# Optimization experiments

Measured on AMD Instinct MI355X. Metric: run time of the kernel, lower is better.

The kernel has to match this reference:

```python
import jax, jax.numpy as jnp
import numpy as np

D = 512        # input_dim
T = 64         # n_trees
DEPTH = 3
NI = 2 ** DEPTH - 1   # 7 internal nodes
NL = 2 ** DEPTH       # 8 leaves
PPT = NI * D + NI + NL * 2   # params per tree
TOT = PPT * T + T            # + tree_weights
HID = 64


def setup_inputs() -> dict:
    key = jax.random.key(0)
    ks = jax.random.split(key, 10)
    w = lambda k, s: jax.random.normal(k, s, jnp.float32) * 0.05  # xavier-ish small gain
    return {
        "X_train": jax.random.normal(ks[0], (8192, D), jnp.float32),
        "X_test": jax.random.normal(ks[1], (32768, D), jnp.float32),
        "y_train": jax.random.randint(ks[2], (8192,), 0, 2, jnp.int64),
        "W1": w(ks[3], (HID, D)), "b1": jnp.zeros(HID), "g1": jnp.ones(HID), "be1": jnp.zeros(HID),
        "W2": w(ks[4], (HID, HID)), "b2": jnp.zeros(HID),
        "H1": w(ks[5], (2 * HID, HID)), "hb1": jnp.zeros(2 * HID),
        "g2": jnp.ones(2 * HID), "be2": jnp.zeros(2 * HID),
        "H2": w(ks[6], (2 * HID, 2 * HID)), "hb2": jnp.zeros(2 * HID),
        "H3": w(ks[7], (TOT, 2 * HID)), "hb3": jnp.zeros(TOT),
    }


def _ln(x, g, b, eps=1e-5):
    m = x.mean(-1, keepdims=True)
    v = ((x - m) ** 2).mean(-1, keepdims=True)
    return (x - m) / jnp.sqrt(v + eps) * g + b


def reference(X_train, X_test, y_train, W1, b1, g1, be1, W2, b2,
              H1, hb1, g2, be2, H2, hb2, H3, hb3):
    # --- hypernet: data encoder + param generator (Dropout is eval=identity) ---
    h = jax.nn.relu(_ln(X_train @ W1.T + b1, g1, be1))
    h = jax.nn.relu(h @ W2.T + b2)
    c = h.mean(axis=0)                              # [HID] context
    u = jax.nn.relu(_ln(c @ H1.T + hb1, g2, be2))
    u = jax.nn.relu(u @ H2.T + hb2)
    params = u @ H3.T + hb3                         # [TOT]

    # --- parse per-tree params (sequential layout) ---
    rows = params[: T * PPT].reshape(T, PPT)
    sw = rows[:, : NI * D].reshape(T, NI, D)        # split weights
    sb = rows[:, NI * D: NI * D + NI]               # split bias [T, NI]
    ll = rows[:, NI * D + NI:].reshape(T, NL, 2)    # leaf logits
    tw = params[T * PPT:]                           # tree weights [T]

    # --- soft decision trees, all trees/nodes batched ---
    # sigmoid split prob for every (sample, tree, internal node); temperature=1
    p = jax.nn.sigmoid(jnp.einsum('bd,tnd->btn', X_test, sw) + sb[None])  # [B,T,NI]
    B = X_test.shape[0]
    lp = jnp.ones((B, T, 1), X_test.dtype)
    for d in range(DEPTH):                          # unrolled fixed-depth traversal
        s = 2 ** d - 1                              # heap offset of level d
        pd = p[:, :, s: s + 2 ** d]                 # [B,T,2^d]
        lp = jnp.stack([lp * (1 - pd), lp * pd], axis=-1).reshape(B, T, 2 ** (d + 1))
    # original code adds leaf contributions twice (main loop + cleanup loop)
    lp = lp * 2.0                                   # [B,T,NL]

    leaf_dist = jax.nn.softmax(ll, axis=-1)         # [T,NL,2]
    out_t = jnp.einsum('btl,tlc->btc', lp, leaf_dist)
    w = jax.nn.softmax(tw, axis=0)                  # [T]
    return jnp.einsum('btc,t->bc', out_t, w)        # [B,2]
```

## Files before the change

### kernel.cpp

```cpp
#include <hip/hip_runtime.h>
#include <hip/hip_bf16.h>

#define DD 512
#define HIDN 64
#define NTREE 64
#define NIN 7
#define PPTC 3607
#define TOTP 230912
#define SWROWS 448

typedef __attribute__((ext_vector_type(8))) short bf16x8;
typedef __attribute__((ext_vector_type(4))) float f32x4;
typedef __attribute__((ext_vector_type(8))) _Float16 h16x8;

__device__ __forceinline__ unsigned short f2bf(float f) {
  unsigned u = __float_as_uint(f);
  unsigned r = (u + 0x7FFFu + ((u >> 16) & 1u)) >> 16;
  return (unsigned short)r;
}
__device__ __forceinline__ float sigmoidf_(float x) {
  return 1.0f / (1.0f + __expf(-x));
}
__device__ __forceinline__ uint2 pack_bf16x4(float4 v) {
  uint2 pk;
  pk.x = (unsigned)f2bf(v.x) | ((unsigned)f2bf(v.y) << 16);
  pk.y = (unsigned)f2bf(v.z) | ((unsigned)f2bf(v.w) << 16);
  return pk;
}
__device__ __forceinline__ bf16x8 cvt8(float4 a, float4 b) {
  unsigned u0, u1, u2, u3;
  asm("v_cvt_pk_bf16_f32 %0, %1, %2" : "=v"(u0) : "v"(a.x), "v"(a.y));
  asm("v_cvt_pk_bf16_f32 %0, %1, %2" : "=v"(u1) : "v"(a.z), "v"(a.w));
  asm("v_cvt_pk_bf16_f32 %0, %1, %2" : "=v"(u2) : "v"(b.x), "v"(b.y));
  asm("v_cvt_pk_bf16_f32 %0, %1, %2" : "=v"(u3) : "v"(b.z), "v"(b.w));
  union { unsigned u[4]; bf16x8 v; } r;
  r.u[0] = u0; r.u[1] = u1; r.u[2] = u2; r.u[3] = u3;
  return r.v;
}

__global__ __launch_bounds__(256) void k_train(
    const float* __restrict__ Xtr, const float* __restrict__ W1,
    const float* __restrict__ b1, const float* __restrict__ g1,
    const float* __restrict__ be1, const float* __restrict__ W2,
    const float* __restrict__ b2, float* __restrict__ c_part)
{
  __shared__ __align__(16) char smem[37888];
  char* Xc  = smem;
  char* W1c = smem + 8192;
  char* Hl  = smem + 24576;
  char* W2l = smem + 28672;
  float* lnb = (float*)(smem + 36864);
  float* cp  = (float*)(smem + 37376);

  const int tid = threadIdx.x;
  const int lane = tid & 63;
  const int wv = tid >> 6;
  const int l15 = lane & 15;
  const int gq = lane >> 4;
  const int wm = wv >> 1;
  const int wn = wv & 1;
  const int rb0 = blockIdx.x * 32;

  const float4* X4g = (const float4*)Xtr;
  const float4* W4g = (const float4*)W1;

#pragma unroll
  for (int s = 0; s < 4; ++s) {
    int fidx = tid + s * 256;
    int n = fidx >> 4, kq = fidx & 15;
    float4 v = ((const float4*)W2)[n * 16 + kq];
    uint2 pk = pack_bf16x4(v);
    int off = n * 128 + kq * 8; off ^= (n & 7) << 4;
    *(uint2*)(W2l + off) = pk;
  }

  int xga[4], xo[4];
#pragma unroll
  for (int s = 0; s < 4; ++s) {
    int f = tid + s * 256;
    int m = f >> 5, kq = f & 31;
    xga[s] = (rb0 + m) * 128 + kq;
    xo[s] = (m * 256 + kq * 8) ^ ((m & 7) << 4);
  }
  int wga[8], wo[8];
#pragma unroll
  for (int s = 0; s < 8; ++s) {
    int f = tid + s * 256;
    int n = f >> 5, kq = f & 31;
    wga[s] = n * 128 + kq;
    wo[s] = (n * 256 + kq * 8) ^ ((n & 7) << 4);
  }

  f32x4 acc1[2];
#pragma unroll
  for (int nt = 0; nt < 2; ++nt) { f32x4 z = {0.f,0.f,0.f,0.f}; acc1[nt] = z; }

  float4 xr[4], wr[8];
#pragma unroll
  for (int s = 0; s < 4; ++s) xr[s] = X4g[xga[s]];
#pragma unroll
  for (int s = 0; s < 8; ++s) wr[s] = W4g[wga[s]];

  for (int kc = 0; kc < 4; ++kc) {
    __syncthreads();
#pragma unroll
    for (int s = 0; s < 4; ++s) *(uint2*)(Xc + xo[s]) = pack_bf16x4(xr[s]);
#pragma unroll
    for (int s = 0; s < 8; ++s) *(uint2*)(W1c + wo[s]) = pack_bf16x4(wr[s]);
    if (kc < 3) {
      int ko = (kc + 1) * 32;
#pragma unroll
      for (int s = 0; s < 4; ++s) xr[s] = X4g[xga[s] + ko];
#pragma unroll
      for (int s = 0; s < 8; ++s) wr[s] = W4g[wga[s] + ko];
    }
    __syncthreads();
#pragma unroll
    for (int ks = 0; ks < 4; ++ks) {
      int arow = wm * 16 + l15;
      int aoff = (arow * 256 + ks * 64 + gq * 16) ^ ((arow & 7) << 4);
      bf16x8 afr = *(const bf16x8*)(Xc + aoff);
#pragma unroll
      for (int nt = 0; nt < 2; ++nt) {
        int brow = wn * 32 + nt * 16 + l15;
        int boff = (brow * 256 + ks * 64 + gq * 16) ^ ((brow & 7) << 4);
        bf16x8 bfr = *(const bf16x8*)(W1c + boff);
        acc1[nt] = __builtin_amdgcn_mfma_f32_16x16x32_bf16(afr, bfr, acc1[nt], 0, 0, 0);
      }
    }
  }

  float b1v[2], g1v[2], be1v[2], b2v[2];
#pragma unroll
  for (int nt = 0; nt < 2; ++nt) {
    int c = wn * 32 + nt * 16 + l15;
    b1v[nt] = b1[c]; g1v[nt] = g1[c]; be1v[nt] = be1[c]; b2v[nt] = b2[c];
  }
  float yv[2][4], s_[4], q_[4];
#pragma unroll
  for (int i = 0; i < 4; ++i) {
    float s = 0.f, q = 0.f;
#pragma unroll
    for (int nt = 0; nt < 2; ++nt) {
      float y = acc1[nt][i] + b1v[nt];
      yv[nt][i] = y; s += y; q += y * y;
    }
    s_[i] = s; q_[i] = q;
  }
#pragma unroll
  for (int off = 1; off < 16; off <<= 1) {
#pragma unroll
    for (int i = 0; i < 4; ++i) {
      s_[i] += __shfl_xor(s_[i], off);
      q_[i] += __shfl_xor(q_[i], off);
    }
  }
  if (l15 == 0) {
#pragma unroll
    for (int i = 0; i < 4; ++i) {
      int row = wm * 16 + gq * 4 + i;
      float2 sv; sv.x = s_[i]; sv.y = q_[i];
      *(float2*)(lnb + (row * 2 + wn) * 2) = sv;
    }
  }
  __syncthreads();
#pragma unroll
  for (int i = 0; i < 4; ++i) {
    int row = wm * 16 + gq * 4 + i;
    float2 e0 = *(float2*)(lnb + (row * 2 + 0) * 2);
    float2 e1 = *(float2*)(lnb + (row * 2 + 1) * 2);
    float m = (e0.x + e1.x) * (1.0f / 64.0f);
    float var = (e0.y + e1.y) * (1.0f / 64.0f) - m * m;
    float rstd = rsqrtf(var + 1e-5f);
#pragma unroll
    for (int nt = 0; nt < 2; ++nt) {
      float h = (yv[nt][i] - m) * rstd * g1v[nt] + be1v[nt];
      h = fmaxf(h, 0.0f);
      int col = wn * 32 + nt * 16 + l15;
      int off2 = (row * 128 + col * 2) ^ ((row & 7) << 4);
      *(unsigned short*)(Hl + off2) = f2bf(h);
    }
  }
  __syncthreads();

  f32x4 acc2[2];
#pragma unroll
  for (int nt = 0; nt < 2; ++nt) { f32x4 z = {0.f,0.f,0.f,0.f}; acc2[nt] = z; }
#pragma unroll
  for (int ks = 0; ks < 2; ++ks) {
    int arow = wm * 16 + l15;
    int aoff = (arow * 128 + ks * 64 + gq * 16) ^ ((arow & 7) << 4);
    bf16x8 afr = *(const bf16x8*)(Hl + aoff);
#pragma unroll
    for (int nt = 0; nt < 2; ++nt) {
      int brow = wn * 32 + nt * 16 + l15;
      int boff = (brow * 128 + ks * 64 + gq * 16) ^ ((brow & 7) << 4);
      bf16x8 bfr = *(const bf16x8*)(W2l + boff);
      acc2[nt] = __builtin_amdgcn_mfma_f32_16x16x32_bf16(afr, bfr, acc2[nt], 0, 0, 0);
    }
  }
  float cs[2];
#pragma unroll
  for (int nt = 0; nt < 2; ++nt) {
    float s = 0.f;
#pragma unroll
    for (int i = 0; i < 4; ++i) s += fmaxf(acc2[nt][i] + b2v[nt], 0.0f);
    cs[nt] = s;
  }
#pragma unroll
  for (int nt = 0; nt < 2; ++nt) {
    cs[nt] += __shfl_xor(cs[nt], 16);
    cs[nt] += __shfl_xor(cs[nt], 32);
  }
  if (lane < 16) {
#pragma unroll
    for (int nt = 0; nt < 2; ++nt)
      cp[wm * 64 + wn * 32 + nt * 16 + lane] = cs[nt];
  }
  __syncthreads();
  if (tid < 64) c_part[blockIdx.x * 64 + tid] = cp[tid] + cp[64 + tid];
}

__global__ __launch_bounds__(256) void k_head(
    const float* __restrict__ c_part,
    const float* __restrict__ H1, const float* __restrict__ hb1,
    const float* __restrict__ g2, const float* __restrict__ be2,
    const float* __restrict__ H2, const float* __restrict__ hb2,
    float* __restrict__ u2out)
{
  __shared__ float part[256];
  __shared__ float clds[64];
  __shared__ float u1lds[128];
  __shared__ float red[8];
  int tid = threadIdx.x;
  {
    int col = tid & 63, g = tid >> 6;
    float s0 = 0.f, s1 = 0.f, s2 = 0.f, s3 = 0.f;
    int b0 = g * 64;
    for (int b = 0; b < 64; b += 4) {
      s0 += c_part[(b0 + b + 0) * 64 + col];
      s1 += c_part[(b0 + b + 1) * 64 + col];
      s2 += c_part[(b0 + b + 2) * 64 + col];
      s3 += c_part[(b0 + b + 3) * 64 + col];
    }
    part[tid] = (s0 + s1) + (s2 + s3);
  }
  __syncthreads();
  if (tid < 64)
    clds[tid] = (part[tid] + part[64 + tid] + part[128 + tid] + part[192 + tid]) * (1.0f / 8192.0f);
  __syncthreads();
  float acc = 0.f;
  if (tid < 128) {
    float a0 = 0.f, a1 = 0.f, a2 = 0.f, a3 = 0.f;
    for (int k = 0; k < 64; k += 4) {
      a0 += clds[k + 0] * H1[tid * 64 + k + 0];
      a1 += clds[k + 1] * H1[tid * 64 + k + 1];
      a2 += clds[k + 2] * H1[tid * 64 + k + 2];
      a3 += clds[k + 3] * H1[tid * 64 + k + 3];
    }
    acc = hb1[tid] + ((a0 + a1) + (a2 + a3));
  }
  float s = acc, q = acc * acc;
#pragma unroll
  for (int off = 1; off < 64; off <<= 1) { s += __shfl_xor(s, off); q += __shfl_xor(q, off); }
  int wv = tid >> 6;
  if ((tid & 63) == 0) { red[wv * 2] = s; red[wv * 2 + 1] = q; }
  __syncthreads();
  float S = red[0] + red[2], Q = red[1] + red[3];
  float m = S * (1.0f / 128.0f);
  float var = Q * (1.0f / 128.0f) - m * m;
  float rstd = rsqrtf(var + 1e-5f);
  if (tid < 128)
    u1lds[tid] = fmaxf((acc - m) * rstd * g2[tid] + be2[tid], 0.0f);
  __syncthreads();
  if (tid < 128) {
    float c0 = 0.f, c1 = 0.f, c2 = 0.f, c3 = 0.f;
    for (int k = 0; k < 128; k += 4) {
      c0 += u1lds[k + 0] * H2[tid * 128 + k + 0];
      c1 += u1lds[k + 1] * H2[tid * 128 + k + 1];
      c2 += u1lds[k + 2] * H2[tid * 128 + k + 2];
      c3 += u1lds[k + 3] * H2[tid * 128 + k + 3];
    }
    u2out[tid] = fmaxf(hb2[tid] + ((c0 + c1) + (c2 + c3)), 0.0f);
  }
}

__global__ __launch_bounds__(256) void k_params(
    const float* __restrict__ H3, const float* __restrict__ hb3,
    const float* __restrict__ u2,
    unsigned short* __restrict__ Bsw, float* __restrict__ sb,
    float* __restrict__ ll, float* __restrict__ tw)
{
  __shared__ float u2l[128];
  int tid = threadIdx.x;
  if (tid < 128) u2l[tid] = u2[tid];
  __syncthreads();
  int row = blockIdx.x * 64 + (tid >> 2);
  int sub = tid & 3;
  float acc = 0.0f;
  const float4* H4 = (const float4*)H3;
#pragma unroll
  for (int j = 0; j < 8; ++j) {
    int f = j * 4 + sub;
    float4 v = H4[row * 32 + f];
    acc += v.x * u2l[f * 4] + v.y * u2l[f * 4 + 1] + v.z * u2l[f * 4 + 2] + v.w * u2l[f * 4 + 3];
  }
  acc += __shfl_xor(acc, 1);
  acc += __shfl_xor(acc, 2);
  if (sub == 0) {
    float val = acc + hb3[row];
    if (row >= 230848) {
      tw[row - 230848] = val;
    } else {
      int t = row / PPTC;
      int r = row - t * PPTC;
      if (r < 3584) {
        int n = r >> 9, d = r & 511;
        Bsw[(t * 7 + n) * 512 + d] = f2bf(val);
      } else if (r < 3591) {
        sb[t * 7 + (r - 3584)] = val;
      } else {
        ll[t * 16 + (r - 3591)] = val;
      }
    }
  }
}

__global__ __launch_bounds__(512) void k_test(
    const float* __restrict__ Xt, const unsigned short* __restrict__ Bsw,
    const float* __restrict__ sb, const float* __restrict__ ll,
    const float* __restrict__ tw, float* __restrict__ out)
{
  __shared__ __align__(16) char smem[64256];
  char* Bb0 = smem;
  char* Bb1 = smem + 28672;
  char* Pl  = smem;
  float* qlds = (float*)(smem + 57344);
  float* sbl  = (float*)(smem + 61440);
  float* outl = (float*)(smem + 63232);

  const int tid = threadIdx.x;
  const int lane = tid & 63;
  const int wv = tid >> 6;
  const int l15 = lane & 15;
  const int gq = lane >> 4;
  const int wm = wv >> 2;
  const int wn = wv & 3;
  const int bm0 = blockIdx.x * 128;
  const bool btail = (tid < 256);

  int bg[4], bo[4];
#pragma unroll
  for (int s = 0; s < 4; ++s) {
    int idx = tid + s * 512;
    int n = idx >> 2, part = idx & 3;
    bg[s] = n * 64 + part;
    bo[s] = (n * 64 + part * 16) ^ ((n & 7) << 4);
  }
  int abase[4];
#pragma unroll
  for (int mt = 0; mt < 4; ++mt) {
    int row = bm0 + wm * 64 + mt * 16 + l15;
    abase[mt] = row * 128 + gq * 2;
  }
  int boffs[7];
#pragma unroll
  for (int nt = 0; nt < 7; ++nt) {
    int r = wn * 112 + nt * 16 + l15;
    boffs[nt] = (r * 64 + gq * 16) ^ ((r & 7) << 4);
  }

  f32x4 acc[4][7];
#pragma unroll
  for (int mt = 0; mt < 4; ++mt)
#pragma unroll
    for (int nt = 0; nt < 7; ++nt) { f32x4 z = {0.f,0.f,0.f,0.f}; acc[mt][nt] = z; }

  const float4* X4 = (const float4*)Xt;
  const uint4* B4 = (const uint4*)Bsw;

  float4 af[4][2];
  bf16x8 abf[4];
  uint4 br0, br1, br2, br3;

#define LOADA(kt) do { _Pragma("unroll") \
    for (int mt = 0; mt < 4; ++mt) { \
      af[mt][0] = X4[abase[mt] + (kt) * 8]; \
      af[mt][1] = X4[abase[mt] + (kt) * 8 + 1]; } } while (0)
#define CVTA() do { _Pragma("unroll") \
    for (int mt = 0; mt < 4; ++mt) abf[mt] = cvt8(af[mt][0], af[mt][1]); } while (0)
#define LOADB(kt) do { \
    br0 = B4[bg[0] + (kt) * 4]; br1 = B4[bg[1] + (kt) * 4]; \
    br2 = B4[bg[2] + (kt) * 4]; if (btail) br3 = B4[bg[3] + (kt) * 4]; } while (0)
#define STOREB(Bb) do { \
    *(uint4*)((Bb) + bo[0]) = br0; *(uint4*)((Bb) + bo[1]) = br1; \
    *(uint4*)((Bb) + bo[2]) = br2; if (btail) *(uint4*)((Bb) + bo[3]) = br3; } while (0)
#define COMPUTE(Bb) do { _Pragma("unroll") \
    for (int nt = 0; nt < 7; ++nt) { \
      bf16x8 bfr = *(const bf16x8*)((Bb) + boffs[nt]); \
      _Pragma("unroll") \
      for (int mt = 0; mt < 4; ++mt) \
        acc[mt][nt] = __builtin_amdgcn_mfma_f32_16x16x32_bf16(abf[mt], bfr, acc[mt][nt], 0, 0, 0); \
    } } while (0)

  LOADA(0);
  LOADB(0);
  STOREB(Bb0);
  LOADB(1);
  if (tid < 448) sbl[tid] = sb[tid];
  if (tid < 64) {
    int t = tid;
    float x = tw[t];
    float m = x;
#pragma unroll
    for (int off = 1; off < 64; off <<= 1) m = fmaxf(m, __shfl_xor(m, off));
    float e = __expf(x - m);
    float s = e;
#pragma unroll
    for (int off = 1; off < 64; off <<= 1) s += __shfl_xor(s, off);
    float w = e / s;
#pragma unroll
    for (int l = 0; l < 8; ++l) {
      float a = ll[t * 16 + l * 2], b = ll[t * 16 + l * 2 + 1];
      float mm = fmaxf(a, b);
      float e0 = __expf(a - mm), e1 = __expf(b - mm);
      float inv = 2.0f * w / (e0 + e1);
      qlds[t * 16 + l * 2] = e0 * inv;
      qlds[t * 16 + l * 2 + 1] = e1 * inv;
    }
  }
  __syncthreads();

  for (int kt2 = 0; kt2 < 16; kt2 += 2) {
    CVTA();
    STOREB(Bb1);
    if (kt2 + 2 < 16) LOADB(kt2 + 2);
    LOADA(kt2 + 1);
    COMPUTE(Bb0);
    __syncthreads();
    CVTA();
    if (kt2 + 2 < 16) {
      STOREB(Bb0);
      if (kt2 + 3 < 16) LOADB(kt2 + 3);
      LOADA(kt2 + 2);
    }
    COMPUTE(Bb1);
    __syncthreads();
  }

  float qreg[16];
  {
    const float4* q4 = (const float4*)qlds;
#pragma unroll
    for (int j = 0; j < 4; ++j) {
      float4 v = q4[lane * 4 + j];
      qreg[j * 4] = v.x; qreg[j * 4 + 1] = v.y; qreg[j * 4 + 2] = v.z; qreg[j * 4 + 3] = v.w;
    }
  }

#pragma unroll
  for (int rg = 0; rg < 4; ++rg) {
    if (wm == (rg >> 1)) {
#pragma unroll
      for (int mtl = 0; mtl < 2; ++mtl) {
        const int mt = (rg & 1) * 2 + mtl;
#pragma unroll
        for (int nt = 0; nt < 7; ++nt) {
          int col = wn * 112 + nt * 16 + l15;
          float sbv = sbl[col];
          int t = col / 7;
          int j = col - t * 7;
          int slot2 = (t * 8 + j) * 2;
#pragma unroll
          for (int i = 0; i < 4; ++i) {
            int rl = mtl * 16 + gq * 4 + i;
            float p = sigmoidf_(acc[mt][nt][i] + sbv);
            *(_Float16*)(Pl + rl * 1024 + slot2) = (_Float16)p;
          }
        }
      }
    }
    __syncthreads();
#pragma unroll
    for (int k = 0; k < 4; ++k) {
      int rl = wv * 4 + k;
      h16x8 v = *(const h16x8*)(Pl + rl * 1024 + lane * 16);
      float p0 = (float)v[0], p1 = (float)v[1], p2 = (float)v[2];
      float p3 = (float)v[3], p4 = (float)v[4], p5 = (float)v[5], p6 = (float)v[6];
      float n0 = 1.f - p0, n1 = 1.f - p1, n2 = 1.f - p2;
      float a00 = n0 * n1, a01 = n0 * p1, a10 = p0 * n2, a11 = p0 * p2;
      float L0 = a00 * (1.f - p3), L1 = a00 * p3;
      float L2 = a01 * (1.f - p4), L3 = a01 * p4;
      float L4 = a10 * (1.f - p5), L5 = a10 * p5;
      float L6 = a11 * (1.f - p6), L7 = a11 * p6;
      float o0 = L0*qreg[0] + L1*qreg[2] + L2*qreg[4] + L3*qreg[6]
               + L4*qreg[8] + L5*qreg[10] + L6*qreg[12] + L7*qreg[14];
      float o1 = L0*qreg[1] + L1*qreg[3] + L2*qreg[5] + L3*qreg[7]
               + L4*qreg[9] + L5*qreg[11] + L6*qreg[13] + L7*qreg[15];
#pragma unroll
      for (int off = 1; off < 64; off <<= 1) {
        o0 += __shfl_xor(o0, off);
        o1 += __shfl_xor(o1, off);
      }
      if (lane == 0) {
        int gr = rg * 32 + rl;
        outl[gr * 2] = o0;
        outl[gr * 2 + 1] = o1;
      }
    }
    __syncthreads();
  }
  if (tid < 256) out[bm0 * 2 + tid] = outl[tid];
#undef LOADA
#undef CVTA
#undef LOADB
#undef STOREB
#undef COMPUTE
}

extern "C" void kernel_launch(void* const* d_in, const int* in_sizes, int n_in,
                              void* d_out, int out_size, void* d_ws, size_t ws_size,
                              hipStream_t stream)
{
  const float* Xtr = (const float*)d_in[0];
  const float* Xte = (const float*)d_in[1];
  const float* W1  = (const float*)d_in[3];
  const float* b1  = (const float*)d_in[4];
  const float* g1  = (const float*)d_in[5];
  const float* be1 = (const float*)d_in[6];
  const float* W2  = (const float*)d_in[7];
  const float* b2  = (const float*)d_in[8];
  const float* H1  = (const float*)d_in[9];
  const float* hb1 = (const float*)d_in[10];
  const float* g2  = (const float*)d_in[11];
  const float* be2 = (const float*)d_in[12];
  const float* H2  = (const float*)d_in[13];
  const float* hb2 = (const float*)d_in[14];
  const float* H3  = (const float*)d_in[15];
  const float* hb3 = (const float*)d_in[16];
  float* out = (float*)d_out;
  char* ws = (char*)d_ws;

  float* c_part = (float*)ws;
  float* u2     = (float*)(ws + 65536);
  float* sb     = (float*)(ws + 66048);
  float* ll     = (float*)(ws + 67840);
  float* tw     = (float*)(ws + 71936);
  unsigned short* Bsw = (unsigned short*)(ws + 72192);

  k_train<<<256, 256, 0, stream>>>(Xtr, W1, b1, g1, be1, W2, b2, c_part);
  k_head<<<1, 256, 0, stream>>>(c_part, H1, hb1, g2, be2, H2, hb2, u2);
  k_params<<<3608, 256, 0, stream>>>(H3, hb3, u2, Bsw, sb, ll, tw);
  k_test<<<256, 512, 0, stream>>>(Xte, Bsw, sb, ll, tw, out);
}
```

Measured before the change: 101.3 us.

## Stream X and split weights into LDS via async global_load_lds triple buffering

Replaces the register-staged double-buffered load loop in the test kernel with direct global-to-LDS async loads (global_load_lds) into a three-stage ring buffer. The X tile is now staged in LDS as fp32 and converted to bf16 at read time, and explicit vmcnt waits control the overlap. The goal is to keep more memory traffic in flight and cut register staging and VGPR pressure. In exchange LDS use per block rises to about 150KB, which allows only one block per CU. The new B layout is unswizzled, so LDS bank conflicts are possible.

Measured after the change: 101.1 us. About the same (-0.2%).

```diff
diff --git a/kernel.cpp b/kernel.cpp
--- a/kernel.cpp
+++ b/kernel.cpp
@@ -36,6 +36,11 @@
   union { unsigned u[4]; bf16x8 v; } r;
   r.u[0] = u0; r.u[1] = u1; r.u[2] = u2; r.u[3] = u3;
   return r.v;
+}
+__device__ __forceinline__ void gl_lds16(const void* g, void* l) {
+  __builtin_amdgcn_global_load_lds(
+      (const __attribute__((address_space(1))) unsigned int*)g,
+      (__attribute__((address_space(3))) unsigned int*)l, 16, 0, 0);
 }
 
 __global__ __launch_bounds__(256) void k_train(
@@ -331,13 +336,11 @@
     const float* __restrict__ sb, const float* __restrict__ ll,
     const float* __restrict__ tw, float* __restrict__ out)
 {
-  __shared__ __align__(16) char smem[64256];
-  char* Bb0 = smem;
-  char* Bb1 = smem + 28672;
-  char* Pl  = smem;
-  float* qlds = (float*)(smem + 57344);
-  float* sbl  = (float*)(smem + 61440);
-  float* outl = (float*)(smem + 63232);
+  __shared__ __align__(16) char smem[154368];
+  char* Pl = smem;
+  float* qlds = (float*)(smem + 147456);
+  float* sbl  = (float*)(smem + 151552);
+  float* outl = (float*)(smem + 153344);
 
   const int tid = threadIdx.x;
   const int lane = tid & 63;
@@ -347,66 +350,10 @@
   const int wm = wv >> 2;
   const int wn = wv & 3;
   const int bm0 = blockIdx.x * 128;
-  const bool btail = (tid < 256);
-
-  int bg[4], bo[4];
-#pragma unroll
-  for (int s = 0; s < 4; ++s) {
-    int idx = tid + s * 512;
-    int n = idx >> 2, part = idx & 3;
-    bg[s] = n * 64 + part;
-    bo[s] = (n * 64 + part * 16) ^ ((n & 7) << 4);
-  }
-  int abase[4];
-#pragma unroll
-  for (int mt = 0; mt < 4; ++mt) {
-    int row = bm0 + wm * 64 + mt * 16 + l15;
-    abase[mt] = row * 128 + gq * 2;
-  }
-  int boffs[7];
-#pragma unroll
-  for (int nt = 0; nt < 7; ++nt) {
-    int r = wn * 112 + nt * 16 + l15;
-    boffs[nt] = (r * 64 + gq * 16) ^ ((r & 7) << 4);
-  }
-
-  f32x4 acc[4][7];
-#pragma unroll
-  for (int mt = 0; mt < 4; ++mt)
-#pragma unroll
-    for (int nt = 0; nt < 7; ++nt) { f32x4 z = {0.f,0.f,0.f,0.f}; acc[mt][nt] = z; }
 
   const float4* X4 = (const float4*)Xt;
   const uint4* B4 = (const uint4*)Bsw;
 
-  float4 af[4][2];
-  bf16x8 abf[4];
-  uint4 br0, br1, br2, br3;
-
-#define LOADA(kt) do { _Pragma("unroll") \
-    for (int mt = 0; mt < 4; ++mt) { \
-      af[mt][0] = X4[abase[mt] + (kt) * 8]; \
-      af[mt][1] = X4[abase[mt] + (kt) * 8 + 1]; } } while (0)
-#define CVTA() do { _Pragma("unroll") \
-    for (int mt = 0; mt < 4; ++mt) abf[mt] = cvt8(af[mt][0], af[mt][1]); } while (0)
-#define LOADB(kt) do { \
-    br0 = B4[bg[0] + (kt) * 4]; br1 = B4[bg[1] + (kt) * 4]; \
-    br2 = B4[bg[2] + (kt) * 4]; if (btail) br3 = B4[bg[3] + (kt) * 4]; } while (0)
-#define STOREB(Bb) do { \
-    *(uint4*)((Bb) + bo[0]) = br0; *(uint4*)((Bb) + bo[1]) = br1; \
-    *(uint4*)((Bb) + bo[2]) = br2; if (btail) *(uint4*)((Bb) + bo[3]) = br3; } while (0)
-#define COMPUTE(Bb) do { _Pragma("unroll") \
-    for (int nt = 0; nt < 7; ++nt) { \
-      bf16x8 bfr = *(const bf16x8*)((Bb) + boffs[nt]); \
-      _Pragma("unroll") \
-      for (int mt = 0; mt < 4; ++mt) \
-        acc[mt][nt] = __builtin_amdgcn_mfma_f32_16x16x32_bf16(abf[mt], bfr, acc[mt][nt], 0, 0, 0); \
-    } } while (0)
-
-  LOADA(0);
-  LOADB(0);
-  STOREB(Bb0);
-  LOADB(1);
   if (tid < 448) sbl[tid] = sb[tid];
   if (tid < 64) {
     int t = tid;
@@ -429,24 +376,73 @@
       qlds[t * 16 + l * 2 + 1] = e1 * inv;
     }
   }
-  __syncthreads();
-
-  for (int kt2 = 0; kt2 < 16; kt2 += 2) {
-    CVTA();
-    STOREB(Bb1);
-    if (kt2 + 2 < 16) LOADB(kt2 + 2);
-    LOADA(kt2 + 1);
-    COMPUTE(Bb0);
-    __syncthreads();
-    CVTA();
-    if (kt2 + 2 < 16) {
-      STOREB(Bb0);
-      if (kt2 + 3 < 16) LOADB(kt2 + 3);
-      LOADA(kt2 + 2);
-    }
-    COMPUTE(Bb1);
-    __syncthreads();
-  }
+
+  const int xkg0 = tid >> 7,         xrow0 = tid & 127;
+  const int xkg1 = (tid + 512) >> 7, xrow1 = tid & 127;
+#define ISSUE_TILE(t_) do { \
+    char* xb_ = smem + ((t_) % 3) * 49152; \
+    char* bb_ = xb_ + 16384; \
+    gl_lds16(X4 + ((bm0 + xrow0) * 128 + (t_) * 8 + xkg0), xb_ + tid * 16); \
+    gl_lds16(X4 + ((bm0 + xrow1) * 128 + (t_) * 8 + xkg1), xb_ + (tid + 512) * 16); \
+    gl_lds16(B4 + (tid * 64 + (t_) * 4 + 0), bb_ + (0 * 512 + tid) * 16); \
+    gl_lds16(B4 + (tid * 64 + (t_) * 4 + 1), bb_ + (1 * 512 + tid) * 16); \
+    gl_lds16(B4 + (tid * 64 + (t_) * 4 + 2), bb_ + (2 * 512 + tid) * 16); \
+    gl_lds16(B4 + (tid * 64 + (t_) * 4 + 3), bb_ + (3 * 512 + tid) * 16); \
+  } while (0)
+
+  f32x4 acc[4][7];
+#pragma unroll
+  for (int mt = 0; mt < 4; ++mt)
+#pragma unroll
+    for (int nt = 0; nt < 7; ++nt) { f32x4 z = {0.f,0.f,0.f,0.f}; acc[mt][nt] = z; }
+
+#define COMPUTE_TILE(t_) do { \
+    char* xb_ = smem + ((t_) % 3) * 49152; \
+    char* bb_ = xb_ + 16384; \
+    bf16x8 abf[4]; \
+    _Pragma("unroll") \
+    for (int mt = 0; mt < 4; ++mt) { \
+      int row = wm * 64 + mt * 16 + l15; \
+      float4 a0 = *(const float4*)(xb_ + ((2 * gq) * 128 + row) * 16); \
+      float4 a1 = *(const float4*)(xb_ + ((2 * gq + 1) * 128 + row) * 16); \
+      abf[mt] = cvt8(a0, a1); \
+    } \
+    _Pragma("unroll") \
+    for (int nt = 0; nt < 7; ++nt) { \
+      int n = wn * 112 + nt * 16 + l15; \
+      bf16x8 bfr = *(const bf16x8*)(bb_ + (gq * 512 + n) * 16); \
+      _Pragma("unroll") \
+      for (int mt = 0; mt < 4; ++mt) \
+        acc[mt][nt] = __builtin_amdgcn_mfma_f32_16x16x32_bf16(abf[mt], bfr, acc[mt][nt], 0, 0, 0); \
+    } } while (0)
+
+  ISSUE_TILE(0);
+  ISSUE_TILE(1);
+  ISSUE_TILE(2);
+
+  for (int t = 0; t < 13; ++t) {
+    asm volatile("s_waitcnt vmcnt(12)" ::: "memory");
+    __builtin_amdgcn_sched_barrier(0);
+    __builtin_amdgcn_s_barrier();
+    COMPUTE_TILE(t);
+    __builtin_amdgcn_s_barrier();
+    ISSUE_TILE(t + 3);
+  }
+  asm volatile("s_waitcnt vmcnt(12)" ::: "memory");
+  __builtin_amdgcn_sched_barrier(0);
+  __builtin_amdgcn_s_barrier();
+  COMPUTE_TILE(13);
+  __builtin_amdgcn_s_barrier();
+  asm volatile("s_waitcnt vmcnt(6)" ::: "memory");
+  __builtin_amdgcn_sched_barrier(0);
+  __builtin_amdgcn_s_barrier();
+  COMPUTE_TILE(14);
+  __builtin_amdgcn_s_barrier();
+  asm volatile("s_waitcnt vmcnt(0)" ::: "memory");
+  __builtin_amdgcn_sched_barrier(0);
+  __builtin_amdgcn_s_barrier();
+  COMPUTE_TILE(15);
+  __syncthreads();
 
   float qreg[16];
   {
@@ -511,11 +507,8 @@
     __syncthreads();
   }
   if (tid < 256) out[bm0 * 2 + tid] = outl[tid];
-#undef LOADA
-#undef CVTA
-#undef LOADB
-#undef STOREB
-#undef COMPUTE
+#undef ISSUE_TILE
+#undef COMPUTE_TILE
 }
 
 extern "C" void kernel_launch(void* const* d_in, const int* in_sizes, int n_in,
```
